# Optimization experiments

Hardware: AMD Instinct MI355X
Metric: run time of the kernel (lower is better)

## Reference

```python
import jax, jax.numpy as jnp
import numpy as np

NB = 4
QN = -(2 ** (NB - 1))   # -8
QP = 2 ** (NB - 1) - 1  # 7
EPS = 1e-5


def _grad_scale(x, g):
    # forward: x, backward: grad * g (LSQ gradient scaling)
    return x * g + jax.lax.stop_gradient(x - x * g)


def _round_pass(x):
    # round with straight-through estimator
    return x + jax.lax.stop_gradient(jnp.round(x) - x)


def _lsq(v, alpha, qn, qp):
    # LSQ fake quantize-dequantize with learnable step size alpha
    g = 1.0 / np.sqrt(v.size * qp)
    a = _grad_scale(alpha, g)
    return _round_pass(jnp.clip(v / a, qn, qp)) * a


def _bn(x, g, b, m, v):
    # eval-mode BatchNorm2d over channel dim of NCHW
    s = (g * jax.lax.rsqrt(v + EPS))[None, :, None, None]
    return (x - m[None, :, None, None]) * s + b[None, :, None, None]


def _conv(x, w, stride, pad, groups):
    return jax.lax.conv_general_dilated(
        x, w, (stride, stride), pad,
        dimension_numbers=('NCHW', 'OIHW', 'NCHW'),
        feature_group_count=groups)


def setup_inputs() -> dict:
    key = jax.random.key(0)
    ks = jax.random.split(key, 4)
    inp, oup, hid = 96, 96, 576
    B, H, W = 32, 28, 28
    d = {}
    d['x'] = jax.random.normal(ks[0], (B, inp, H, W), jnp.float32)
    d['w1'] = jax.random.normal(ks[1], (hid, inp, 1, 1), jnp.float32) * 0.1
    d['w2'] = jax.random.normal(ks[2], (hid, 1, 3, 3), jnp.float32) * 0.1
    d['w3'] = jax.random.normal(ks[3], (oup, hid, 1, 1), jnp.float32) * 0.1
    for i, c in zip((1, 2, 3), (hid, hid, oup)):
        d[f'aw{i}'] = jnp.full((1,), 0.05, jnp.float32)  # weight step size
        d[f'ax{i}'] = jnp.full((1,), 0.5, jnp.float32)   # activation step size
        d[f'g{i}'] = jnp.ones((c,), jnp.float32)
        d[f'b{i}'] = jnp.zeros((c,), jnp.float32)
        d[f'm{i}'] = jnp.zeros((c,), jnp.float32)
        d[f'v{i}'] = jnp.ones((c,), jnp.float32)
    return d


def reference(x, w1, w2, w3, aw1, ax1, g1, b1, m1, v1,
              aw2, ax2, g2, b2, m2, v2, aw3, ax3, g3, b3, m3, v3):
    hid = w1.shape[0]
    # 1x1 expand conv (LSQ on activation and weight)
    h = _conv(_lsq(x, ax1, QN, QP), _lsq(w1, aw1, QN, QP), 1, [(0, 0), (0, 0)], 1)
    h = jnp.clip(_bn(h, g1, b1, m1, v1), 0.0, 6.0)
    # 3x3 depthwise conv, stride 1
    h = _conv(_lsq(h, ax2, QN, QP), _lsq(w2, aw2, QN, QP), 1, [(1, 1), (1, 1)], hid)
    h = jnp.clip(_bn(h, g2, b2, m2, v2), 0.0, 6.0)
    # 1x1 project conv
    h = _conv(_lsq(h, ax3, QN, QP), _lsq(w3, aw3, QN, QP), 1, [(0, 0), (0, 0)], 1)
    h = _bn(h, g3, b3, m3, v3)
    # identity residual (stride==1 and inp==oup)
    return x + h
```

## Files before the change

### kernel.cpp

```cpp
#include <hip/hip_runtime.h>

#define EPSF 1e-5f

typedef int    int4v   __attribute__((ext_vector_type(4)));
typedef float  float4v __attribute__((ext_vector_type(4)));

#define W1P_OFF  0
#define W3P_OFF  55296
#define W2D_OFF  110592
#define S1B1_OFF 202752
#define S2B2_OFF 207360
#define S3B3_OFF 211968

#define H1S 296
#define H2S 296

__device__ __forceinline__ float lsq_q(float v, float a) {
    float t = v / a;
    t = fminf(fmaxf(t, -8.0f), 7.0f);
    return rintf(t);
}

__device__ __forceinline__ long q8pack_w(const float* w, int base, float a) {
    unsigned long long v = 0;
    #pragma unroll
    for (int j = 0; j < 8; ++j) {
        int q = (int)lsq_q(w[base + j], a);
        v |= (unsigned long long)(q & 255) << (8 * j);
    }
    return (long)v;
}

__device__ __forceinline__ long q8pack_wp(const float* w, int base, const int* idx, float a) {
    unsigned long long v = 0;
    #pragma unroll
    for (int j = 0; j < 8; ++j) {
        int q = (int)lsq_q(w[base + idx[j]], a);
        v |= (unsigned long long)(q & 255) << (8 * j);
    }
    return (long)v;
}

__global__ __launch_bounds__(256)
void prep_w(const float* __restrict__ w1, const float* __restrict__ w2,
            const float* __restrict__ w3,
            const float* aw1, const float* ax1, const float* ax2,
            const float* aw2, const float* ax3, const float* aw3,
            const float* __restrict__ g1, const float* __restrict__ b1,
            const float* __restrict__ m1, const float* __restrict__ v1,
            const float* __restrict__ g2, const float* __restrict__ b2,
            const float* __restrict__ m2, const float* __restrict__ v2,
            const float* __restrict__ g3, const float* __restrict__ b3,
            const float* __restrict__ m3, const float* __restrict__ v3,
            long* __restrict__ w1p, long* __restrict__ w3p,
            long* __restrict__ w2d,
            float* __restrict__ s1b1, float* __restrict__ s2b2,
            float* __restrict__ s3b3) {
    int id = blockIdx.x * 256 + threadIdx.x;
    if (id < 6912) {
        int l = id & 63, t = id >> 6;
        int kc = t % 3, ct = t / 3;
        int co = ct * 16 + (l & 15);
        int ci0 = kc * 32 + (l >> 4) * 8;
        w1p[id] = q8pack_w(w1, co * 96 + ci0, aw1[0]);
    } else if (id < 13824) {
        int i = id - 6912;
        int l = i & 63, t = i >> 6;
        int kc = t % 18, ct = t / 18;
        int co = ct * 16 + (l & 15);
        int ci0 = kc * 32 + (l >> 4) * 8;
        const int perm[8] = {0, 2, 4, 6, 1, 3, 5, 7};
        w3p[i] = q8pack_wp(w3, co * 576 + ci0, perm, aw3[0]);
    } else if (id < 25344) {
        int i = id - 13824;
        int l = i & 63, t = i >> 6;
        int kc = t % 5, ct = t / 5;
        int quad = l >> 4, m = l & 15;
        int tap = kc * 2 + (quad >> 1);
        unsigned long long v = 0;
        if (tap <= 8) {
            int mh = m - (quad & 1) * 8;
            if (mh >= 0 && mh < 8) {
                int j = (mh >> 1) | ((mh & 1) << 2);
                int q = (int)lsq_q(w2[(ct * 16 + m) * 9 + tap], aw2[0]);
                v = (unsigned long long)(unsigned)(q & 255) << (8 * j);
            }
        }
        w2d[i] = (long)v;
    } else if (id < 25920) {
        int c = id - 25344;
        float s = g1[c] / sqrtf(v1[c] + EPSF);
        float A = aw1[0] * ax1[0];
        float inv = 1.0f / ax2[0];
        s1b1[c] = A * s * inv;
        s1b1[576 + c] = (b1[c] - m1[c] * s) * inv;
    } else if (id < 26496) {
        int c = id - 25920;
        float s = g2[c] / sqrtf(v2[c] + EPSF);
        float A = ax2[0] * aw2[0];
        float inv = 1.0f / ax3[0];
        s2b2[c] = A * s * inv;
        s2b2[576 + c] = (b2[c] - m2[c] * s) * inv;
    } else if (id < 26592) {
        int c = id - 26496;
        float s = g3[c] / sqrtf(v3[c] + EPSF);
        float A = ax3[0] * aw3[0];
        s3b3[c] = A * s;
        s3b3[96 + c] = b3[c] - m3[c] * s;
    }
}

__global__ __launch_bounds__(448, 7)
void fused_k(const float* __restrict__ x, const long* __restrict__ w1p,
             const long* __restrict__ w2d, const long* __restrict__ w3p,
             const float* __restrict__ ax1,
             const float* __restrict__ s1b1, const float* __restrict__ s2b2,
             const float* __restrict__ s3b3, float* __restrict__ out) {
    __shared__ unsigned char h1[90 * H1S];
    __shared__ unsigned char h2[32 * H2S];
    const int tid = threadIdx.x;
    const int w = tid >> 6, l = tid & 63;
    const int quad = l >> 4, c16 = l & 15;
    const int qh = quad >> 1, ql = quad & 1;
    const int b = blockIdx.x;
    const int r = blockIdx.y;

    if (w < 6) {
        const int sp = w * 16 + c16;
        const int tr = sp / 28, col = sp - tr * 28;
        const int ir = r - 1 + tr;
        const bool vrow = (unsigned)ir < 28u;
        const bool vpos = sp < 84;
        const int p = min(max(ir, 0), 27) * 28 + col;
        const float inv1 = 1.0f / ax1[0];

        long bfr[3];
        #pragma unroll
        for (int kc = 0; kc < 3; ++kc) {
            const float* xs = x + (b * 96 + kc * 32 + quad * 8) * 784 + p;
            unsigned long long v = 0;
            #pragma unroll
            for (int j = 0; j < 8; ++j) {
                float t = xs[j * 784] * inv1;
                t = fminf(fmaxf(t, -8.0f), 7.0f);
                int q = (int)rintf(t);
                v |= (unsigned long long)(q & 255) << (8 * j);
            }
            bfr[kc] = (long)v;
        }
        const int pos_h = tr * 30 + col + 1;
        #pragma unroll 4
        for (int ct = 0; ct < 36; ++ct) {
            int4v acc; acc[0] = 0; acc[1] = 0; acc[2] = 0; acc[3] = 0;
            #pragma unroll
            for (int kc = 0; kc < 3; ++kc)
                acc = __builtin_amdgcn_mfma_i32_16x16x32_i8(
                    w1p[(ct * 3 + kc) * 64 + l], bfr[kc], acc, 0, 0, 0);
            const int co0 = ct * 16 + quad * 4;
            float4v S = *(const float4v*)(s1b1 + co0);
            float4v B = *(const float4v*)(s1b1 + 576 + co0);
            int pk = 0;
            #pragma unroll
            for (int rr = 0; rr < 4; ++rr) {
                float t = fmaf((float)acc[rr], S[rr], B[rr]);
                t = fminf(fmaxf(t, 0.0f), 7.0f);
                pk |= ((int)rintf(t)) << (4 * rr);
            }
            pk = vrow ? pk : 0;
            if (vpos)
                *(unsigned short*)(h1 + pos_h * H1S + ct * 8 + quad * 2) = (unsigned short)pk;
        }
    }
    if (tid < 432) {
        const int tr = tid / 144, rem = tid - tr * 144;
        const int colh = (rem / 72) * 29, word = rem - (rem / 72) * 72;
        *(int*)(h1 + (tr * 30 + colh) * H1S + word * 4) = 0;
    }
    __syncthreads();

    int boff[5];
    #pragma unroll
    for (int kc = 0; kc < 5; ++kc) {
        int tap = kc * 2 + qh;
        tap = min(tap, 8);
        const int dh = tap / 3 - 1, dc = tap - (tap / 3) * 3 - 1;
        boff[kc] = (dh * 30 + dc) * H1S;
    }
    for (int t = w; t < 72; t += 7) {
        const int pt = (t >= 36) ? 1 : 0, ct = t - pt * 36;
        const int pos = pt * 16 + c16;
        const int col = min(pos, 27);
        const unsigned char* sbase = h1 + (30 + col + 1) * H1S + ct * 8 + ql * 4;
        int4v acc; acc[0] = 0; acc[1] = 0; acc[2] = 0; acc[3] = 0;
        #pragma unroll
        for (int kc = 0; kc < 5; ++kc) {
            const unsigned v = *(const unsigned*)(sbase + boff[kc]);
            const long bf = (long)((((unsigned long long)((v >> 4) & 0x0F0F0F0Fu)) << 32)
                                   | (v & 0x0F0F0F0Fu));
            acc = __builtin_amdgcn_mfma_i32_16x16x32_i8(
                w2d[(ct * 5 + kc) * 64 + l], bf, acc, 0, 0, 0);
        }
        const int c0 = ct * 16 + quad * 4;
        float4v S = *(const float4v*)(s2b2 + c0);
        float4v B = *(const float4v*)(s2b2 + 576 + c0);
        int pk = 0;
        #pragma unroll
        for (int rr = 0; rr < 4; ++rr) {
            float tt = fmaf((float)acc[rr], S[rr], B[rr]);
            tt = fminf(fmaxf(tt, 0.0f), 7.0f);
            pk |= ((int)rintf(tt)) << (4 * rr);
        }
        if (pos < 28)
            *(unsigned short*)(h2 + pos * H2S + ct * 8 + quad * 2) = (unsigned short)pk;
    }
    __syncthreads();

    for (int t = w; t < 12; t += 7) {
        const int nt = t / 6, ct = t - nt * 6;
        const unsigned char* arow = h2 + (nt * 16 + c16) * H2S + quad * 4;
        int4v acc; acc[0] = 0; acc[1] = 0; acc[2] = 0; acc[3] = 0;
        #pragma unroll 6
        for (int kc = 0; kc < 18; ++kc) {
            const unsigned v = *(const unsigned*)(arow + kc * 16);
            const long a = (long)((((unsigned long long)((v >> 4) & 0x0F0F0F0Fu)) << 32)
                                  | (v & 0x0F0F0F0Fu));
            acc = __builtin_amdgcn_mfma_i32_16x16x32_i8(
                a, w3p[(ct * 18 + kc) * 64 + l], acc, 0, 0, 0);
        }
        const int nloc = nt * 16 + quad * 4;
        if (nloc < 28) {
            const int co = ct * 16 + c16;
            const float S = s3b3[co], Bv = s3b3[96 + co];
            const int off = (b * 96 + co) * 784 + r * 28 + nloc;
            const float4v xr = *(const float4v*)(x + off);
            float4v o;
            #pragma unroll
            for (int rr = 0; rr < 4; ++rr)
                o[rr] = fmaf((float)acc[rr], S, Bv) + xr[rr];
            *(float4v*)(out + off) = o;
        }
    }
}

extern "C" void kernel_launch(void* const* d_in, const int* in_sizes, int n_in,
                              void* d_out, int out_size, void* d_ws, size_t ws_size,
                              hipStream_t stream) {
    const float* x   = (const float*)d_in[0];
    const float* w1  = (const float*)d_in[1];
    const float* w2  = (const float*)d_in[2];
    const float* w3  = (const float*)d_in[3];
    const float* aw1 = (const float*)d_in[4];
    const float* ax1 = (const float*)d_in[5];
    const float* g1  = (const float*)d_in[6];
    const float* b1  = (const float*)d_in[7];
    const float* m1  = (const float*)d_in[8];
    const float* v1  = (const float*)d_in[9];
    const float* aw2 = (const float*)d_in[10];
    const float* ax2 = (const float*)d_in[11];
    const float* g2  = (const float*)d_in[12];
    const float* b2  = (const float*)d_in[13];
    const float* m2  = (const float*)d_in[14];
    const float* v2  = (const float*)d_in[15];
    const float* aw3 = (const float*)d_in[16];
    const float* ax3 = (const float*)d_in[17];
    const float* g3  = (const float*)d_in[18];
    const float* b3  = (const float*)d_in[19];
    const float* m3  = (const float*)d_in[20];
    const float* v3  = (const float*)d_in[21];

    char* ws = (char*)d_ws;
    long* w1p = (long*)(ws + W1P_OFF);
    long* w3p = (long*)(ws + W3P_OFF);
    long* w2d = (long*)(ws + W2D_OFF);
    float* s1b1 = (float*)(ws + S1B1_OFF);
    float* s2b2 = (float*)(ws + S2B2_OFF);
    float* s3b3 = (float*)(ws + S3B3_OFF);

    float* out = (float*)d_out;

    prep_w<<<104, 256, 0, stream>>>(w1, w2, w3, aw1, ax1, ax2, aw2, ax3, aw3,
                                    g1, b1, m1, v1, g2, b2, m2, v2, g3, b3, m3, v3,
                                    w1p, w3p, w2d, s1b1, s2b2, s3b3);
    dim3 grid(32, 28);
    fused_k<<<grid, 448, 0, stream>>>(x, w1p, w2d, w3p, ax1, s1b1, s2b2, s3b3, out);
}
```

Before: 162.3 us.

## Split fused block kernel into expand+depthwise and separate projection kernels

The single fused kernel is replaced by two kernels. The first computes the 1x1 expand conv and the 3x3 depthwise conv for two output rows and half the hidden channels per block, then writes packed 4-bit depthwise outputs to a global workspace. The second kernel runs the 1x1 projection with the residual add over 16-pixel tiles. This cuts the halo recomputation of the expand conv (three input rows per output row down to two per output row) and lets each kernel get its own occupancy. The cost is an extra global round trip for the intermediate activations and a second launch, and the uncoalesced 2-byte gathers in the projection kernel may be slow.

```diff
diff --git a/kernel.cpp b/kernel.cpp
--- a/kernel.cpp
+++ b/kernel.cpp
@@ -5,15 +5,15 @@
 typedef int    int4v   __attribute__((ext_vector_type(4)));
 typedef float  float4v __attribute__((ext_vector_type(4)));
 
-#define W1P_OFF  0
-#define W3P_OFF  55296
-#define W2D_OFF  110592
-#define S1B1_OFF 202752
-#define S2B2_OFF 207360
-#define S3B3_OFF 211968
-
-#define H1S 296
-#define H2S 296
+#define QH2S_OFF 0
+#define W1P_OFF  7225344
+#define W3P_OFF  7280640
+#define W2D_OFF  7335936
+#define S1B1_OFF 7428096
+#define S2B2_OFF 7432704
+#define S3B3_OFF 7437312
+
+#define H1S 152
 
 __device__ __forceinline__ float lsq_q(float v, float a) {
     float t = v / a;
@@ -110,28 +110,26 @@
     }
 }
 
-__global__ __launch_bounds__(448, 7)
-void fused_k(const float* __restrict__ x, const long* __restrict__ w1p,
-             const long* __restrict__ w2d, const long* __restrict__ w3p,
-             const float* __restrict__ ax1,
-             const float* __restrict__ s1b1, const float* __restrict__ s2b2,
-             const float* __restrict__ s3b3, float* __restrict__ out) {
-    __shared__ unsigned char h1[90 * H1S];
-    __shared__ unsigned char h2[32 * H2S];
+__global__ __launch_bounds__(448, 4)
+void c1dw_k(const float* __restrict__ x, const long* __restrict__ w1p,
+            const long* __restrict__ w2d, const float* __restrict__ ax1,
+            const float* __restrict__ s1b1, const float* __restrict__ s2b2,
+            unsigned short* __restrict__ qh2s) {
+    __shared__ unsigned char h1[120 * H1S];
     const int tid = threadIdx.x;
     const int w = tid >> 6, l = tid & 63;
     const int quad = l >> 4, c16 = l & 15;
     const int qh = quad >> 1, ql = quad & 1;
     const int b = blockIdx.x;
-    const int r = blockIdx.y;
-
-    if (w < 6) {
-        const int sp = w * 16 + c16;
-        const int tr = sp / 28, col = sp - tr * 28;
-        const int ir = r - 1 + tr;
-        const bool vrow = (unsigned)ir < 28u;
-        const bool vpos = sp < 84;
-        const int p = min(max(ir, 0), 27) * 28 + col;
+    const int r0 = blockIdx.y * 2;
+    const int ctb = blockIdx.z * 18;
+
+    {
+        const int lp = w * 16 + c16;
+        const int row = lp / 28, col = lp - (lp / 28) * 28;
+        const int img_row = r0 - 1 + row;
+        const bool vrow = (unsigned)img_row < 28u;
+        const int p = min(max(img_row, 0), 27) * 28 + col;
         const float inv1 = 1.0f / ax1[0];
 
         long bfr[3];
@@ -148,9 +146,10 @@
             }
             bfr[kc] = (long)v;
         }
-        const int pos_h = tr * 30 + col + 1;
-        #pragma unroll 4
-        for (int ct = 0; ct < 36; ++ct) {
+        const int pos_h = row * 30 + col + 1;
+        #pragma unroll 3
+        for (int ctl = 0; ctl < 18; ++ctl) {
+            const int ct = ctb + ctl;
             int4v acc; acc[0] = 0; acc[1] = 0; acc[2] = 0; acc[3] = 0;
             #pragma unroll
             for (int kc = 0; kc < 3; ++kc)
@@ -167,14 +166,13 @@
                 pk |= ((int)rintf(t)) << (4 * rr);
             }
             pk = vrow ? pk : 0;
-            if (vpos)
-                *(unsigned short*)(h1 + pos_h * H1S + ct * 8 + quad * 2) = (unsigned short)pk;
-        }
-    }
-    if (tid < 432) {
-        const int tr = tid / 144, rem = tid - tr * 144;
-        const int colh = (rem / 72) * 29, word = rem - (rem / 72) * 72;
-        *(int*)(h1 + (tr * 30 + colh) * H1S + word * 4) = 0;
+            *(unsigned short*)(h1 + pos_h * H1S + ctl * 8 + quad * 2) = (unsigned short)pk;
+        }
+    }
+    if (tid < 304) {
+        const int q = tid / 38, word = tid - q * 38;
+        const int pos_h = (q >> 1) * 30 + (q & 1) * 29;
+        *(int*)(h1 + pos_h * H1S + word * 4) = 0;
     }
     __syncthreads();
 
@@ -187,10 +185,12 @@
         boff[kc] = (dh * 30 + dc) * H1S;
     }
     for (int t = w; t < 72; t += 7) {
-        const int pt = (t >= 36) ? 1 : 0, ct = t - pt * 36;
+        const int pt = t / 18, ctl = t - pt * 18;
+        const int ct = ctb + ctl;
         const int pos = pt * 16 + c16;
-        const int col = min(pos, 27);
-        const unsigned char* sbase = h1 + (30 + col + 1) * H1S + ct * 8 + ql * 4;
+        const int pc = min(pos, 55);
+        const int rA = pc / 28, cA = pc - rA * 28;
+        const unsigned char* sbase = h1 + ((rA + 1) * 30 + cA + 1) * H1S + ctl * 8 + ql * 4;
         int4v acc; acc[0] = 0; acc[1] = 0; acc[2] = 0; acc[3] = 0;
         #pragma unroll
         for (int kc = 0; kc < 5; ++kc) {
@@ -210,36 +210,45 @@
             tt = fminf(fmaxf(tt, 0.0f), 7.0f);
             pk |= ((int)rintf(tt)) << (4 * rr);
         }
-        if (pos < 28)
-            *(unsigned short*)(h2 + pos * H2S + ct * 8 + quad * 2) = (unsigned short)pk;
-    }
-    __syncthreads();
-
-    for (int t = w; t < 12; t += 7) {
-        const int nt = t / 6, ct = t - nt * 6;
-        const unsigned char* arow = h2 + (nt * 16 + c16) * H2S + quad * 4;
-        int4v acc; acc[0] = 0; acc[1] = 0; acc[2] = 0; acc[3] = 0;
-        #pragma unroll 6
-        for (int kc = 0; kc < 18; ++kc) {
-            const unsigned v = *(const unsigned*)(arow + kc * 16);
-            const long a = (long)((((unsigned long long)((v >> 4) & 0x0F0F0F0Fu)) << 32)
-                                  | (v & 0x0F0F0F0Fu));
-            acc = __builtin_amdgcn_mfma_i32_16x16x32_i8(
-                a, w3p[(ct * 18 + kc) * 64 + l], acc, 0, 0, 0);
-        }
-        const int nloc = nt * 16 + quad * 4;
-        if (nloc < 28) {
-            const int co = ct * 16 + c16;
-            const float S = s3b3[co], Bv = s3b3[96 + co];
-            const int off = (b * 96 + co) * 784 + r * 28 + nloc;
-            const float4v xr = *(const float4v*)(x + off);
-            float4v o;
-            #pragma unroll
-            for (int rr = 0; rr < 4; ++rr)
-                o[rr] = fmaf((float)acc[rr], S, Bv) + xr[rr];
-            *(float4v*)(out + off) = o;
-        }
-    }
+        if (pos < 56)
+            qh2s[(ct * 4 + quad) * 25088 + b * 784 + r0 * 28 + pos] = (unsigned short)pk;
+    }
+}
+
+__global__ __launch_bounds__(384, 4)
+void conv3_k(const unsigned short* __restrict__ qh2s, const long* __restrict__ w3p,
+             const float* __restrict__ x, const float* __restrict__ s3b3,
+             float* __restrict__ out) {
+    const int tid = threadIdx.x;
+    const int w = tid >> 6, l = tid & 63;
+    const int quad = l >> 4, c16 = l & 15;
+    const int n0 = blockIdx.x * 16;
+    const int n = n0 + c16;
+
+    int4v acc; acc[0] = 0; acc[1] = 0; acc[2] = 0; acc[3] = 0;
+    #pragma unroll 6
+    for (int kc = 0; kc < 18; ++kc) {
+        const int s0 = kc * 8 + quad * 2;
+        const unsigned u0 = qh2s[s0 * 25088 + n];
+        const unsigned u1 = qh2s[(s0 + 1) * 25088 + n];
+        const unsigned v = u0 | (u1 << 16);
+        const long a = (long)((((unsigned long long)((v >> 4) & 0x0F0F0F0Fu)) << 32)
+                              | (v & 0x0F0F0F0Fu));
+        acc = __builtin_amdgcn_mfma_i32_16x16x32_i8(
+            a, w3p[(w * 18 + kc) * 64 + l], acc, 0, 0, 0);
+    }
+
+    const int co = w * 16 + c16;
+    const float S = s3b3[co], Bv = s3b3[96 + co];
+    const int nb = n0 + quad * 4;
+    const int bi = nb / 784, p0 = nb - bi * 784;
+    const int off = (bi * 96 + co) * 784 + p0;
+    const float4v xr = *(const float4v*)(x + off);
+    float4v o;
+    #pragma unroll
+    for (int rr = 0; rr < 4; ++rr)
+        o[rr] = fmaf((float)acc[rr], S, Bv) + xr[rr];
+    *(float4v*)(out + off) = o;
 }
 
 extern "C" void kernel_launch(void* const* d_in, const int* in_sizes, int n_in,
@@ -269,6 +278,7 @@
     const float* v3  = (const float*)d_in[21];
 
     char* ws = (char*)d_ws;
+    unsigned short* qh2s = (unsigned short*)(ws + QH2S_OFF);
     long* w1p = (long*)(ws + W1P_OFF);
     long* w3p = (long*)(ws + W3P_OFF);
     long* w2d = (long*)(ws + W2D_OFF);
@@ -281,6 +291,7 @@
     prep_w<<<104, 256, 0, stream>>>(w1, w2, w3, aw1, ax1, ax2, aw2, ax3, aw3,
                                     g1, b1, m1, v1, g2, b2, m2, v2, g3, b3, m3, v3,
                                     w1p, w3p, w2d, s1b1, s2b2, s3b3);
-    dim3 grid(32, 28);
-    fused_k<<<grid, 448, 0, stream>>>(x, w1p, w2d, w3p, ax1, s1b1, s2b2, s3b3, out);
-}
+    dim3 g1d(32, 14, 2);
+    c1dw_k<<<g1d, 448, 0, stream>>>(x, w1p, w2d, ax1, s1b1, s2b2, qh2s);
+    conv3_k<<<1568, 384, 0, stream>>>(qh2s, w3p, x, s3b3, out);
+}
```

New measurement: 157.5 us. 1.03x faster.
